# Optimization experiments

Hardware: AMD Instinct MI355X
Metric: run time of the kernel (lower is better)

The kernel has to match this reference:

```python
import jax, jax.numpy as jnp
import numpy as np

N_EDGES = 1_600_000
D_FEAT = 32
N_NODES = 50_000


def setup_inputs() -> dict:
    key = jax.random.key(0)
    k1, k2, k3, k4 = jax.random.split(key, 4)
    m = jax.random.normal(k1, (N_EDGES, D_FEAT), dtype=jnp.float32)
    dst = jax.random.randint(k2, (N_EDGES,), 0, N_NODES, dtype=jnp.int64)
    w = jax.random.normal(k3, (4,), dtype=jnp.float32)
    b = jax.random.normal(k4, (1,), dtype=jnp.float32)
    return {"m": m, "dst": dst, "w": w, "b": b, "n_nodes": N_NODES}


def reference(m, dst, w, b, n_nodes):
    # Four segment reductions edge->node over destination index (copy_e_*)
    s = jax.ops.segment_sum(m, dst, num_segments=n_nodes)            # [N, D]
    mn = jax.ops.segment_min(m, dst, num_segments=n_nodes)
    mx = jax.ops.segment_max(m, dst, num_segments=n_nodes)
    deg = jax.ops.segment_sum(jnp.ones((m.shape[0],), m.dtype), dst,
                              num_segments=n_nodes)                  # [N]
    has = (deg > 0)[:, None]
    # DGL returns 0 for zero-degree nodes
    mn = jnp.where(has, mn, 0.0)
    mx = jnp.where(has, mx, 0.0)
    mean = s / jnp.maximum(deg, 1.0)[:, None]
    stacked = jnp.stack([s, mn, mx, mean], axis=-1)                  # [N, D, 4]
    out = jnp.einsum('ndk,k->nd', stacked, w) + b[0]                 # Dense(4,1) + squeeze
    return out
```

## Files before the change

### kernel.cpp

```cpp
#include <hip/hip_runtime.h>
#include <math.h>

#define D_FEAT 32
#define BSHIFT 7
#define NODES_PER_BKT 128
#define TILE 8192
#define PT 32
#define MAXBKT 512
#define CAPG 5120
#define GBLK 512

__global__ __launch_bounds__(256) void hist_kernel(const int* __restrict__ dst,
                                                   int* __restrict__ bucketCount,
                                                   int E4, int nbucket) {
    __shared__ int h[MAXBKT];
    for (int i = threadIdx.x; i < MAXBKT; i += 256) h[i] = 0;
    __syncthreads();
    const int4* dst4 = (const int4*)dst;
    int tbase4 = blockIdx.x * (TILE / 4);
    #pragma unroll
    for (int k = 0; k < PT / 4; k++) {
        int i4 = tbase4 + k * 256 + threadIdx.x;
        if (i4 < E4) {
            int4 d = dst4[i4];
            atomicAdd(&h[d.x >> BSHIFT], 1);
            atomicAdd(&h[d.y >> BSHIFT], 1);
            atomicAdd(&h[d.z >> BSHIFT], 1);
            atomicAdd(&h[d.w >> BSHIFT], 1);
        }
    }
    __syncthreads();
    for (int i = threadIdx.x; i < nbucket; i += 256) {
        int c = h[i];
        if (c) atomicAdd(&bucketCount[i], c);
    }
}

__global__ __launch_bounds__(256) void scan_kernel(const int* __restrict__ bucketCount,
                                                   int* __restrict__ bucketBase,
                                                   int* __restrict__ bucketCursor,
                                                   int nbucket, int E) {
    __shared__ int lds[256];
    int tid = threadIdx.x;
    int v0 = bucketCount[2 * tid];
    int v1 = bucketCount[2 * tid + 1];
    int s = v0 + v1;
    lds[tid] = s;
    __syncthreads();
    for (int off = 1; off < 256; off <<= 1) {
        int t = (tid >= off) ? lds[tid - off] : 0;
        __syncthreads();
        lds[tid] += t;
        __syncthreads();
    }
    int run = lds[tid] - s;
    bucketBase[2 * tid] = run;       bucketCursor[2 * tid] = run;
    bucketBase[2 * tid + 1] = run + v0; bucketCursor[2 * tid + 1] = run + v0;
    if (tid == 255) bucketBase[512] = run + s;
}

__global__ __launch_bounds__(256) void partition_kernel(const int* __restrict__ dst,
                                                        int* __restrict__ bucketCursor,
                                                        unsigned int* __restrict__ keys,
                                                        int E4, int nbucket) {
    __shared__ int h[MAXBKT];
    __shared__ int hoff[MAXBKT + 1];
    __shared__ int gbase[MAXBKT];
    __shared__ int scanb[256];
    __shared__ unsigned int stage[TILE];
    int tid = threadIdx.x;
    for (int i = tid; i < MAXBKT; i += 256) h[i] = 0;
    __syncthreads();
    const int4* dst4 = (const int4*)dst;
    int tbase4 = blockIdx.x * (TILE / 4);
    #pragma unroll
    for (int k = 0; k < PT / 4; k++) {
        int i4 = tbase4 + k * 256 + tid;
        if (i4 < E4) {
            int4 d = dst4[i4];
            atomicAdd(&h[d.x >> BSHIFT], 1);
            atomicAdd(&h[d.y >> BSHIFT], 1);
            atomicAdd(&h[d.z >> BSHIFT], 1);
            atomicAdd(&h[d.w >> BSHIFT], 1);
        }
    }
    __syncthreads();
    int v0 = h[2 * tid], v1 = h[2 * tid + 1];
    int s = v0 + v1;
    scanb[tid] = s;
    __syncthreads();
    for (int off = 1; off < 256; off <<= 1) {
        int t = (tid >= off) ? scanb[tid - off] : 0;
        __syncthreads();
        scanb[tid] += t;
        __syncthreads();
    }
    int run = scanb[tid] - s;
    hoff[2 * tid] = run;
    hoff[2 * tid + 1] = run + v0;
    if (tid == 255) hoff[512] = run + s;
    for (int i = tid; i < nbucket; i += 256) {
        int c = h[i];
        gbase[i] = c ? atomicAdd(&bucketCursor[i], c) : 0;
    }
    __syncthreads();
    for (int i = tid; i < MAXBKT; i += 256) h[i] = hoff[i];
    __syncthreads();
    #pragma unroll
    for (int k = 0; k < PT / 4; k++) {
        int i4 = tbase4 + k * 256 + tid;
        if (i4 < E4) {
            int4 d = dst4[i4];
            int e = i4 * 4;
            int r;
            r = atomicAdd(&h[d.x >> BSHIFT], 1);
            stage[r] = ((unsigned)(d.x & (NODES_PER_BKT - 1)) << 21) | (unsigned)e;
            r = atomicAdd(&h[d.y >> BSHIFT], 1);
            stage[r] = ((unsigned)(d.y & (NODES_PER_BKT - 1)) << 21) | (unsigned)(e + 1);
            r = atomicAdd(&h[d.z >> BSHIFT], 1);
            stage[r] = ((unsigned)(d.z & (NODES_PER_BKT - 1)) << 21) | (unsigned)(e + 2);
            r = atomicAdd(&h[d.w >> BSHIFT], 1);
            stage[r] = ((unsigned)(d.w & (NODES_PER_BKT - 1)) << 21) | (unsigned)(e + 3);
        }
    }
    __syncthreads();
    for (int i = tid; i < nbucket; i += 256) {
        int lo = hoff[i], hi = hoff[i + 1];
        int g = gbase[i];
        for (int j = lo; j < hi; j++) keys[g + (j - lo)] = stage[j];
    }
}

__global__ __launch_bounds__(GBLK) void bucket_gather_kernel(
        const float* __restrict__ m,
        const unsigned int* __restrict__ keys,
        const int* __restrict__ bucketBase,
        const float* __restrict__ w,
        const float* __restrict__ bia,
        float* __restrict__ out, int N) {
    __shared__ int seid[CAPG];
    __shared__ int nh[NODES_PER_BKT];
    __shared__ int noff[NODES_PER_BKT + 1];
    __shared__ int ncur[NODES_PER_BKT];
    int bkt = blockIdx.x;
    int tid = threadIdx.x;
    int start = bucketBase[bkt];
    int cnt = bucketBase[bkt + 1] - start;
    if (cnt > CAPG) cnt = CAPG;

    for (int i = tid; i < NODES_PER_BKT; i += GBLK) nh[i] = 0;
    __syncthreads();
    for (int i = tid; i < cnt; i += GBLK)
        atomicAdd(&nh[keys[start + i] >> 21], 1);
    __syncthreads();
    if (tid < 64) {
        int a0 = nh[2 * tid], a1 = nh[2 * tid + 1];
        int s = a0 + a1;
        int x = s;
        #pragma unroll
        for (int off = 1; off < 64; off <<= 1) {
            int t = __shfl_up(x, off, 64);
            if (tid >= off) x += t;
        }
        int base = x - s;
        noff[2 * tid] = base;      ncur[2 * tid] = base;
        noff[2 * tid + 1] = base + a0; ncur[2 * tid + 1] = base + a0;
        if (tid == 63) noff[NODES_PER_BKT] = x;
    }
    __syncthreads();
    for (int i = tid; i < cnt; i += GBLK) {
        unsigned int k = keys[start + i];
        int pos = atomicAdd(&ncur[k >> 21], 1);
        seid[pos] = (int)(k & 0x1FFFFFu);
    }
    __syncthreads();

    const int fo  = tid & 7;
    const int grp = tid >> 3;
    const float w0 = w[0], w1 = w[1], w2 = w[2], w3 = w[3], bb = bia[0];

    for (int nl = grp; nl < NODES_PER_BKT; nl += 64) {
        int node = (bkt << BSHIFT) + nl;
        if (node >= N) break;
        int s0 = noff[nl];     if (s0 > cnt) s0 = cnt;
        int e0 = noff[nl + 1]; if (e0 > cnt) e0 = cnt;
        int deg = e0 - s0;
        float sa0 = 0.f, sa1 = 0.f, sa2 = 0.f, sa3 = 0.f;
        float mn0 = INFINITY, mn1 = INFINITY, mn2 = INFINITY, mn3 = INFINITY;
        float mx0 = -INFINITY, mx1 = -INFINITY, mx2 = -INFINITY, mx3 = -INFINITY;

#define ACC(v)                                                      \
        sa0 += (v).x; mn0 = fminf(mn0, (v).x); mx0 = fmaxf(mx0, (v).x); \
        sa1 += (v).y; mn1 = fminf(mn1, (v).y); mx1 = fmaxf(mx1, (v).y); \
        sa2 += (v).z; mn2 = fminf(mn2, (v).z); mx2 = fmaxf(mx2, (v).z); \
        sa3 += (v).w; mn3 = fminf(mn3, (v).w); mx3 = fmaxf(mx3, (v).w);

        int j = s0;
        for (; j + 4 <= e0; j += 4) {
            int ea = seid[j], eb = seid[j + 1], ec = seid[j + 2], ed = seid[j + 3];
            float4 va = *(const float4*)&m[ea * D_FEAT + (fo << 2)];
            float4 vb = *(const float4*)&m[eb * D_FEAT + (fo << 2)];
            float4 vc = *(const float4*)&m[ec * D_FEAT + (fo << 2)];
            float4 vd = *(const float4*)&m[ed * D_FEAT + (fo << 2)];
            ACC(va); ACC(vb); ACC(vc); ACC(vd);
        }
        for (; j < e0; j++) {
            float4 v = *(const float4*)&m[seid[j] * D_FEAT + (fo << 2)];
            ACC(v);
        }
#undef ACC

        bool has = deg > 0;
        float inv = 1.0f / fmaxf((float)deg, 1.0f);
        float4 o;
        o.x = w0 * sa0 + w1 * (has ? mn0 : 0.f) + w2 * (has ? mx0 : 0.f) + w3 * (sa0 * inv) + bb;
        o.y = w0 * sa1 + w1 * (has ? mn1 : 0.f) + w2 * (has ? mx1 : 0.f) + w3 * (sa1 * inv) + bb;
        o.z = w0 * sa2 + w1 * (has ? mn2 : 0.f) + w2 * (has ? mx2 : 0.f) + w3 * (sa2 * inv) + bb;
        o.w = w0 * sa3 + w1 * (has ? mn3 : 0.f) + w2 * (has ? mx3 : 0.f) + w3 * (sa3 * inv) + bb;
        *(float4*)&out[node * D_FEAT + (fo << 2)] = o;
    }
}

extern "C" void kernel_launch(void* const* d_in, const int* in_sizes, int n_in,
                              void* d_out, int out_size, void* d_ws, size_t ws_size,
                              hipStream_t stream) {
    const float* m   = (const float*)d_in[0];
    const int*   dst = (const int*)  d_in[1];
    const float* w   = (const float*)d_in[2];
    const float* b   = (const float*)d_in[3];

    int E = in_sizes[0] / D_FEAT;
    int N = out_size    / D_FEAT;
    int E4 = E / 4;
    int nbucket = (N + NODES_PER_BKT - 1) >> BSHIFT;

    int* ws           = (int*)d_ws;
    int* bucketCount  = ws;
    int* bucketBase   = bucketCount + MAXBKT;
    int* bucketCursor = bucketBase + MAXBKT + 1;
    unsigned int* keys = (unsigned int*)(bucketCursor + MAXBKT);

    int nTiles = (E + TILE - 1) / TILE;

    hipMemsetAsync(bucketCount, 0, MAXBKT * sizeof(int), stream);
    hipLaunchKernelGGL(hist_kernel, dim3(nTiles), dim3(256), 0, stream,
                       dst, bucketCount, E4, nbucket);
    hipLaunchKernelGGL(scan_kernel, dim3(1), dim3(256), 0, stream,
                       bucketCount, bucketBase, bucketCursor, nbucket, E);
    hipLaunchKernelGGL(partition_kernel, dim3(nTiles), dim3(256), 0, stream,
                       dst, bucketCursor, keys, E4, nbucket);
    hipLaunchKernelGGL(bucket_gather_kernel, dim3(nbucket), dim3(GBLK), 0, stream,
                       m, keys, bucketBase, w, b, (float*)d_out, N);
}
```

Measured before the change: 329.2 us.

## Halve bucket size to 64 nodes and parallelize key scatter per wavefront

Buckets now cover 64 nodes instead of 128, which doubles the number of gather blocks (about 782) and shrinks each block to 256 threads for better occupancy and load balance. The partition kernel's final copy from shared staging to global keys uses one wavefront per bucket with lanes striding, instead of one thread walking each bucket serially, so writes coalesce. The gather kernel caches the keys in shared memory so they are read from global only once. The trade-off is twice as many bucket histogram bins and atomics in the partition pass, plus extra shared memory per gather block. The per-block edge cap CAPG is halved, which risks silently dropping edges if a bucket holds more than 2560.

Measured after the change: 364.8 us. 1.11x slower.

```diff
diff --git a/kernel.cpp b/kernel.cpp
--- a/kernel.cpp
+++ b/kernel.cpp
@@ -2,13 +2,12 @@
 #include <math.h>
 
 #define D_FEAT 32
-#define BSHIFT 7
-#define NODES_PER_BKT 128
+#define BSHIFT 6
+#define NPB 64
 #define TILE 8192
 #define PT 32
-#define MAXBKT 512
-#define CAPG 5120
-#define GBLK 512
+#define MAXBKT 1024
+#define CAPG 2560
 
 __global__ __launch_bounds__(256) void hist_kernel(const int* __restrict__ dst,
                                                    int* __restrict__ bucketCount,
@@ -42,9 +41,10 @@
                                                    int nbucket, int E) {
     __shared__ int lds[256];
     int tid = threadIdx.x;
-    int v0 = bucketCount[2 * tid];
-    int v1 = bucketCount[2 * tid + 1];
-    int s = v0 + v1;
+    int b4 = tid << 2;
+    int v0 = bucketCount[b4], v1 = bucketCount[b4 + 1],
+        v2 = bucketCount[b4 + 2], v3 = bucketCount[b4 + 3];
+    int s = v0 + v1 + v2 + v3;
     lds[tid] = s;
     __syncthreads();
     for (int off = 1; off < 256; off <<= 1) {
@@ -54,9 +54,11 @@
         __syncthreads();
     }
     int run = lds[tid] - s;
-    bucketBase[2 * tid] = run;       bucketCursor[2 * tid] = run;
-    bucketBase[2 * tid + 1] = run + v0; bucketCursor[2 * tid + 1] = run + v0;
-    if (tid == 255) bucketBase[512] = run + s;
+    bucketBase[b4] = run;           bucketCursor[b4] = run;
+    bucketBase[b4 + 1] = run + v0;  bucketCursor[b4 + 1] = run + v0;
+    bucketBase[b4 + 2] = run + v0 + v1;      bucketCursor[b4 + 2] = run + v0 + v1;
+    bucketBase[b4 + 3] = run + v0 + v1 + v2; bucketCursor[b4 + 3] = run + v0 + v1 + v2;
+    if (tid == 255) bucketBase[MAXBKT] = run + s;
 }
 
 __global__ __launch_bounds__(256) void partition_kernel(const int* __restrict__ dst,
@@ -85,8 +87,9 @@
         }
     }
     __syncthreads();
-    int v0 = h[2 * tid], v1 = h[2 * tid + 1];
-    int s = v0 + v1;
+    int b4 = tid << 2;
+    int v0 = h[b4], v1 = h[b4 + 1], v2 = h[b4 + 2], v3 = h[b4 + 3];
+    int s = v0 + v1 + v2 + v3;
     scanb[tid] = s;
     __syncthreads();
     for (int off = 1; off < 256; off <<= 1) {
@@ -96,9 +99,11 @@
         __syncthreads();
     }
     int run = scanb[tid] - s;
-    hoff[2 * tid] = run;
-    hoff[2 * tid + 1] = run + v0;
-    if (tid == 255) hoff[512] = run + s;
+    hoff[b4] = run;
+    hoff[b4 + 1] = run + v0;
+    hoff[b4 + 2] = run + v0 + v1;
+    hoff[b4 + 3] = run + v0 + v1 + v2;
+    if (tid == 255) hoff[MAXBKT] = run + s;
     for (int i = tid; i < nbucket; i += 256) {
         int c = h[i];
         gbase[i] = c ? atomicAdd(&bucketCursor[i], c) : 0;
@@ -114,62 +119,67 @@
             int e = i4 * 4;
             int r;
             r = atomicAdd(&h[d.x >> BSHIFT], 1);
-            stage[r] = ((unsigned)(d.x & (NODES_PER_BKT - 1)) << 21) | (unsigned)e;
+            stage[r] = ((unsigned)(d.x & (NPB - 1)) << 21) | (unsigned)e;
             r = atomicAdd(&h[d.y >> BSHIFT], 1);
-            stage[r] = ((unsigned)(d.y & (NODES_PER_BKT - 1)) << 21) | (unsigned)(e + 1);
+            stage[r] = ((unsigned)(d.y & (NPB - 1)) << 21) | (unsigned)(e + 1);
             r = atomicAdd(&h[d.z >> BSHIFT], 1);
-            stage[r] = ((unsigned)(d.z & (NODES_PER_BKT - 1)) << 21) | (unsigned)(e + 2);
+            stage[r] = ((unsigned)(d.z & (NPB - 1)) << 21) | (unsigned)(e + 2);
             r = atomicAdd(&h[d.w >> BSHIFT], 1);
-            stage[r] = ((unsigned)(d.w & (NODES_PER_BKT - 1)) << 21) | (unsigned)(e + 3);
-        }
-    }
-    __syncthreads();
-    for (int i = tid; i < nbucket; i += 256) {
+            stage[r] = ((unsigned)(d.w & (NPB - 1)) << 21) | (unsigned)(e + 3);
+        }
+    }
+    __syncthreads();
+    int lane = tid & 63;
+    int wv = tid >> 6;
+    for (int i = wv; i < nbucket; i += 4) {
         int lo = hoff[i], hi = hoff[i + 1];
         int g = gbase[i];
-        for (int j = lo; j < hi; j++) keys[g + (j - lo)] = stage[j];
-    }
-}
-
-__global__ __launch_bounds__(GBLK) void bucket_gather_kernel(
+        for (int j = lo + lane; j < hi; j += 64)
+            keys[g + (j - lo)] = stage[j];
+    }
+}
+
+__global__ __launch_bounds__(256) void bucket_gather_kernel(
         const float* __restrict__ m,
         const unsigned int* __restrict__ keys,
         const int* __restrict__ bucketBase,
         const float* __restrict__ w,
         const float* __restrict__ bia,
         float* __restrict__ out, int N) {
+    __shared__ unsigned int ukey[CAPG];
     __shared__ int seid[CAPG];
-    __shared__ int nh[NODES_PER_BKT];
-    __shared__ int noff[NODES_PER_BKT + 1];
-    __shared__ int ncur[NODES_PER_BKT];
+    __shared__ int nh[NPB];
+    __shared__ int noff[NPB + 1];
+    __shared__ int ncur[NPB];
     int bkt = blockIdx.x;
     int tid = threadIdx.x;
     int start = bucketBase[bkt];
     int cnt = bucketBase[bkt + 1] - start;
     if (cnt > CAPG) cnt = CAPG;
 
-    for (int i = tid; i < NODES_PER_BKT; i += GBLK) nh[i] = 0;
-    __syncthreads();
-    for (int i = tid; i < cnt; i += GBLK)
-        atomicAdd(&nh[keys[start + i] >> 21], 1);
+    if (tid < NPB) nh[tid] = 0;
+    __syncthreads();
+    for (int i = tid; i < cnt; i += 256) {
+        unsigned int k = keys[start + i];
+        ukey[i] = k;
+        atomicAdd(&nh[k >> 21], 1);
+    }
     __syncthreads();
     if (tid < 64) {
-        int a0 = nh[2 * tid], a1 = nh[2 * tid + 1];
-        int s = a0 + a1;
-        int x = s;
+        int v = nh[tid];
+        int x = v;
         #pragma unroll
         for (int off = 1; off < 64; off <<= 1) {
             int t = __shfl_up(x, off, 64);
             if (tid >= off) x += t;
         }
-        int base = x - s;
-        noff[2 * tid] = base;      ncur[2 * tid] = base;
-        noff[2 * tid + 1] = base + a0; ncur[2 * tid + 1] = base + a0;
-        if (tid == 63) noff[NODES_PER_BKT] = x;
-    }
-    __syncthreads();
-    for (int i = tid; i < cnt; i += GBLK) {
-        unsigned int k = keys[start + i];
+        noff[tid + 1] = x;
+        if (tid == 0) noff[0] = 0;
+        ncur[tid] = x - v;
+    }
+    __syncthreads();
+    for (int i = tid; i < cnt; i += 256) {
+        unsigned int k = ukey[i];
         int pos = atomicAdd(&ncur[k >> 21], 1);
         seid[pos] = (int)(k & 0x1FFFFFu);
     }
@@ -179,11 +189,11 @@
     const int grp = tid >> 3;
     const float w0 = w[0], w1 = w[1], w2 = w[2], w3 = w[3], bb = bia[0];
 
-    for (int nl = grp; nl < NODES_PER_BKT; nl += 64) {
+    for (int nl = grp; nl < NPB; nl += 32) {
         int node = (bkt << BSHIFT) + nl;
         if (node >= N) break;
-        int s0 = noff[nl];     if (s0 > cnt) s0 = cnt;
-        int e0 = noff[nl + 1]; if (e0 > cnt) e0 = cnt;
+        int s0 = noff[nl];
+        int e0 = noff[nl + 1];
         int deg = e0 - s0;
         float sa0 = 0.f, sa1 = 0.f, sa2 = 0.f, sa3 = 0.f;
         float mn0 = INFINITY, mn1 = INFINITY, mn2 = INFINITY, mn3 = INFINITY;
@@ -232,7 +242,7 @@
     int E = in_sizes[0] / D_FEAT;
     int N = out_size    / D_FEAT;
     int E4 = E / 4;
-    int nbucket = (N + NODES_PER_BKT - 1) >> BSHIFT;
+    int nbucket = (N + NPB - 1) >> BSHIFT;
 
     int* ws           = (int*)d_ws;
     int* bucketCount  = ws;
@@ -249,6 +259,6 @@
                        bucketCount, bucketBase, bucketCursor, nbucket, E);
     hipLaunchKernelGGL(partition_kernel, dim3(nTiles), dim3(256), 0, stream,
                        dst, bucketCursor, keys, E4, nbucket);
-    hipLaunchKernelGGL(bucket_gather_kernel, dim3(nbucket), dim3(GBLK), 0, stream,
+    hipLaunchKernelGGL(bucket_gather_kernel, dim3(nbucket), dim3(256), 0, stream,
                        m, keys, bucketBase, w, b, (float*)d_out, N);
 }
```

## Store per-tile bucket histograms and precompute per-tile offsets in scan

Applied to the files above, without the earlier changes.

The hist kernel now writes each tile's full bucket histogram to workspace instead of atomically adding into global counts. The single-block scan computes both the global bucket bases and every tile's per-bucket starting offset. The partition kernel loads these instead of recomputing its histogram and claiming ranges with global atomics. This removes the second pass over dst, the global atomics and the memset. In exchange the scan block serially walks about 196 tiles per bucket, reading and writing per-tile arrays.

Measured after the change: 343.9 us. 4.5% more time.

```diff
diff --git a/kernel.cpp b/kernel.cpp
--- a/kernel.cpp
+++ b/kernel.cpp
@@ -3,7 +3,7 @@
 
 #define D_FEAT 32
 #define BSHIFT 7
-#define NODES_PER_BKT 128
+#define NPB 128
 #define TILE 8192
 #define PT 32
 #define MAXBKT 512
@@ -11,8 +11,7 @@
 #define GBLK 512
 
 __global__ __launch_bounds__(256) void hist_kernel(const int* __restrict__ dst,
-                                                   int* __restrict__ bucketCount,
-                                                   int E4, int nbucket) {
+                                                   int* __restrict__ tileCnt, int E4) {
     __shared__ int h[MAXBKT];
     for (int i = threadIdx.x; i < MAXBKT; i += 256) h[i] = 0;
     __syncthreads();
@@ -30,37 +29,49 @@
         }
     }
     __syncthreads();
-    for (int i = threadIdx.x; i < nbucket; i += 256) {
-        int c = h[i];
-        if (c) atomicAdd(&bucketCount[i], c);
-    }
-}
-
-__global__ __launch_bounds__(256) void scan_kernel(const int* __restrict__ bucketCount,
+    int t = blockIdx.x;
+    for (int i = threadIdx.x; i < MAXBKT; i += 256)
+        tileCnt[t * MAXBKT + i] = h[i];
+}
+
+__global__ __launch_bounds__(512) void scan_kernel(const int* __restrict__ tileCnt,
+                                                   int* __restrict__ tileBase,
                                                    int* __restrict__ bucketBase,
-                                                   int* __restrict__ bucketCursor,
-                                                   int nbucket, int E) {
-    __shared__ int lds[256];
-    int tid = threadIdx.x;
-    int v0 = bucketCount[2 * tid];
-    int v1 = bucketCount[2 * tid + 1];
-    int s = v0 + v1;
-    lds[tid] = s;
-    __syncthreads();
-    for (int off = 1; off < 256; off <<= 1) {
-        int t = (tid >= off) ? lds[tid - off] : 0;
-        __syncthreads();
-        lds[tid] += t;
-        __syncthreads();
-    }
-    int run = lds[tid] - s;
-    bucketBase[2 * tid] = run;       bucketCursor[2 * tid] = run;
-    bucketBase[2 * tid + 1] = run + v0; bucketCursor[2 * tid + 1] = run + v0;
-    if (tid == 255) bucketBase[512] = run + s;
+                                                   int nTiles) {
+    __shared__ int lds[512];
+    int b = threadIdx.x;
+    int total = 0;
+    int t = 0;
+    #pragma unroll 4
+    for (; t + 4 <= nTiles; t += 4) {
+        int c0 = tileCnt[(t + 0) * MAXBKT + b];
+        int c1 = tileCnt[(t + 1) * MAXBKT + b];
+        int c2 = tileCnt[(t + 2) * MAXBKT + b];
+        int c3 = tileCnt[(t + 3) * MAXBKT + b];
+        total += c0 + c1 + c2 + c3;
+    }
+    for (; t < nTiles; t++) total += tileCnt[t * MAXBKT + b];
+    lds[b] = total;
+    __syncthreads();
+    for (int off = 1; off < 512; off <<= 1) {
+        int v = (b >= off) ? lds[b - off] : 0;
+        __syncthreads();
+        lds[b] += v;
+        __syncthreads();
+    }
+    int base = lds[b] - total;
+    bucketBase[b] = base;
+    if (b == 511) bucketBase[512] = lds[511];
+    int run = base;
+    for (t = 0; t < nTiles; t++) {
+        tileBase[t * MAXBKT + b] = run;
+        run += tileCnt[t * MAXBKT + b];
+    }
 }
 
 __global__ __launch_bounds__(256) void partition_kernel(const int* __restrict__ dst,
-                                                        int* __restrict__ bucketCursor,
+                                                        const int* __restrict__ tileCnt,
+                                                        const int* __restrict__ tileBase,
                                                         unsigned int* __restrict__ keys,
                                                         int E4, int nbucket) {
     __shared__ int h[MAXBKT];
@@ -69,20 +80,10 @@
     __shared__ int scanb[256];
     __shared__ unsigned int stage[TILE];
     int tid = threadIdx.x;
-    for (int i = tid; i < MAXBKT; i += 256) h[i] = 0;
-    __syncthreads();
-    const int4* dst4 = (const int4*)dst;
-    int tbase4 = blockIdx.x * (TILE / 4);
-    #pragma unroll
-    for (int k = 0; k < PT / 4; k++) {
-        int i4 = tbase4 + k * 256 + tid;
-        if (i4 < E4) {
-            int4 d = dst4[i4];
-            atomicAdd(&h[d.x >> BSHIFT], 1);
-            atomicAdd(&h[d.y >> BSHIFT], 1);
-            atomicAdd(&h[d.z >> BSHIFT], 1);
-            atomicAdd(&h[d.w >> BSHIFT], 1);
-        }
+    int t = blockIdx.x;
+    for (int i = tid; i < MAXBKT; i += 256) {
+        h[i] = tileCnt[t * MAXBKT + i];
+        gbase[i] = tileBase[t * MAXBKT + i];
     }
     __syncthreads();
     int v0 = h[2 * tid], v1 = h[2 * tid + 1];
@@ -90,22 +91,20 @@
     scanb[tid] = s;
     __syncthreads();
     for (int off = 1; off < 256; off <<= 1) {
-        int t = (tid >= off) ? scanb[tid - off] : 0;
-        __syncthreads();
-        scanb[tid] += t;
+        int tt = (tid >= off) ? scanb[tid - off] : 0;
+        __syncthreads();
+        scanb[tid] += tt;
         __syncthreads();
     }
     int run = scanb[tid] - s;
     hoff[2 * tid] = run;
     hoff[2 * tid + 1] = run + v0;
-    if (tid == 255) hoff[512] = run + s;
-    for (int i = tid; i < nbucket; i += 256) {
-        int c = h[i];
-        gbase[i] = c ? atomicAdd(&bucketCursor[i], c) : 0;
-    }
+    if (tid == 255) hoff[MAXBKT] = run + s;
     __syncthreads();
     for (int i = tid; i < MAXBKT; i += 256) h[i] = hoff[i];
     __syncthreads();
+    const int4* dst4 = (const int4*)dst;
+    int tbase4 = t * (TILE / 4);
     #pragma unroll
     for (int k = 0; k < PT / 4; k++) {
         int i4 = tbase4 + k * 256 + tid;
@@ -114,13 +113,13 @@
             int e = i4 * 4;
             int r;
             r = atomicAdd(&h[d.x >> BSHIFT], 1);
-            stage[r] = ((unsigned)(d.x & (NODES_PER_BKT - 1)) << 21) | (unsigned)e;
+            stage[r] = ((unsigned)(d.x & (NPB - 1)) << 21) | (unsigned)e;
             r = atomicAdd(&h[d.y >> BSHIFT], 1);
-            stage[r] = ((unsigned)(d.y & (NODES_PER_BKT - 1)) << 21) | (unsigned)(e + 1);
+            stage[r] = ((unsigned)(d.y & (NPB - 1)) << 21) | (unsigned)(e + 1);
             r = atomicAdd(&h[d.z >> BSHIFT], 1);
-            stage[r] = ((unsigned)(d.z & (NODES_PER_BKT - 1)) << 21) | (unsigned)(e + 2);
+            stage[r] = ((unsigned)(d.z & (NPB - 1)) << 21) | (unsigned)(e + 2);
             r = atomicAdd(&h[d.w >> BSHIFT], 1);
-            stage[r] = ((unsigned)(d.w & (NODES_PER_BKT - 1)) << 21) | (unsigned)(e + 3);
+            stage[r] = ((unsigned)(d.w & (NPB - 1)) << 21) | (unsigned)(e + 3);
         }
     }
     __syncthreads();
@@ -139,16 +138,16 @@
         const float* __restrict__ bia,
         float* __restrict__ out, int N) {
     __shared__ int seid[CAPG];
-    __shared__ int nh[NODES_PER_BKT];
-    __shared__ int noff[NODES_PER_BKT + 1];
-    __shared__ int ncur[NODES_PER_BKT];
+    __shared__ int nh[NPB];
+    __shared__ int noff[NPB + 1];
+    __shared__ int ncur[NPB];
     int bkt = blockIdx.x;
     int tid = threadIdx.x;
     int start = bucketBase[bkt];
     int cnt = bucketBase[bkt + 1] - start;
     if (cnt > CAPG) cnt = CAPG;
 
-    for (int i = tid; i < NODES_PER_BKT; i += GBLK) nh[i] = 0;
+    for (int i = tid; i < NPB; i += GBLK) nh[i] = 0;
     __syncthreads();
     for (int i = tid; i < cnt; i += GBLK)
         atomicAdd(&nh[keys[start + i] >> 21], 1);
@@ -165,7 +164,7 @@
         int base = x - s;
         noff[2 * tid] = base;      ncur[2 * tid] = base;
         noff[2 * tid + 1] = base + a0; ncur[2 * tid + 1] = base + a0;
-        if (tid == 63) noff[NODES_PER_BKT] = x;
+        if (tid == 63) noff[NPB] = x;
     }
     __syncthreads();
     for (int i = tid; i < cnt; i += GBLK) {
@@ -179,7 +178,7 @@
     const int grp = tid >> 3;
     const float w0 = w[0], w1 = w[1], w2 = w[2], w3 = w[3], bb = bia[0];
 
-    for (int nl = grp; nl < NODES_PER_BKT; nl += 64) {
+    for (int nl = grp; nl < NPB; nl += 64) {
         int node = (bkt << BSHIFT) + nl;
         if (node >= N) break;
         int s0 = noff[nl];     if (s0 > cnt) s0 = cnt;
@@ -232,23 +231,21 @@
     int E = in_sizes[0] / D_FEAT;
     int N = out_size    / D_FEAT;
     int E4 = E / 4;
-    int nbucket = (N + NODES_PER_BKT - 1) >> BSHIFT;
-
-    int* ws           = (int*)d_ws;
-    int* bucketCount  = ws;
-    int* bucketBase   = bucketCount + MAXBKT;
-    int* bucketCursor = bucketBase + MAXBKT + 1;
-    unsigned int* keys = (unsigned int*)(bucketCursor + MAXBKT);
-
+    int nbucket = (N + NPB - 1) >> BSHIFT;
     int nTiles = (E + TILE - 1) / TILE;
 
-    hipMemsetAsync(bucketCount, 0, MAXBKT * sizeof(int), stream);
+    int* ws         = (int*)d_ws;
+    int* tileCnt    = ws;
+    int* tileBase   = tileCnt  + nTiles * MAXBKT;
+    int* bucketBase = tileBase + nTiles * MAXBKT;
+    unsigned int* keys = (unsigned int*)(bucketBase + MAXBKT + 1);
+
     hipLaunchKernelGGL(hist_kernel, dim3(nTiles), dim3(256), 0, stream,
-                       dst, bucketCount, E4, nbucket);
-    hipLaunchKernelGGL(scan_kernel, dim3(1), dim3(256), 0, stream,
-                       bucketCount, bucketBase, bucketCursor, nbucket, E);
+                       dst, tileCnt, E4);
+    hipLaunchKernelGGL(scan_kernel, dim3(1), dim3(512), 0, stream,
+                       tileCnt, tileBase, bucketBase, nTiles);
     hipLaunchKernelGGL(partition_kernel, dim3(nTiles), dim3(256), 0, stream,
-                       dst, bucketCursor, keys, E4, nbucket);
+                       dst, tileCnt, tileBase, keys, E4, nbucket);
     hipLaunchKernelGGL(bucket_gather_kernel, dim3(nbucket), dim3(GBLK), 0, stream,
                        m, keys, bucketBase, w, b, (float*)d_out, N);
 }
```
